# Kernel optimization log

Hardware: AMD Instinct MI355X
Metric: run time of the kernel (lower is better)

Reference implementation:

```python
import jax, jax.numpy as jnp
import numpy as np

B, H, L, DH = 4, 16, 2048, 64
EMBED_DIM = H * DH
CAUSAL = True


def setup_inputs() -> dict:
    key = jax.random.key(0)
    kq, kk, kv = jax.random.split(key, 3)
    return {
        "query": jax.random.normal(kq, (B, H, L, DH), dtype=jnp.float32),
        "key": jax.random.normal(kk, (B, H, L, DH), dtype=jnp.float32),
        "value": jax.random.normal(kv, (B, H, L, DH), dtype=jnp.float32),
    }


def reference(query, key, value):
    # scaled dot-product attention with causal mask, inputs [B, H, L, Dh]
    scale = 1.0 / jnp.sqrt(jnp.asarray(query.shape[-1], query.dtype))
    scores = jnp.einsum("bhld,bhsd->bhls", query, key) * scale  # [B,H,L,S]
    if CAUSAL:
        q_idx = jnp.arange(query.shape[-2])[:, None]
        k_idx = jnp.arange(key.shape[-2])[None, :]
        neg_inf = jnp.asarray(-jnp.inf, scores.dtype)
        scores = jnp.where(k_idx > q_idx, neg_inf, scores)
    attn = jax.nn.softmax(scores, axis=-1)
    out = jnp.einsum("bhls,bhsd->bhld", attn, value)  # [B,H,L,Dh]
    # merge heads -> [B, L, D]
    b = out.shape[0]
    return out.transpose(0, 2, 1, 3).reshape(b, -1, EMBED_DIM)
```

## Files before the change

kernel.cpp:

```cpp
#include <hip/hip_runtime.h>
#include <hip/hip_bf16.h>

#define B_   4
#define H_   16
#define L_   2048
#define DH_  64
#define QSCALE 0.1803368801111204f
#define LDK  72

typedef __bf16 bf16;
typedef __bf16 bf16x4 __attribute__((ext_vector_type(4)));
typedef __bf16 bf16x8 __attribute__((ext_vector_type(8)));
typedef float  f32x4  __attribute__((ext_vector_type(4)));

typedef const __attribute__((address_space(1))) unsigned int* gptr_t;
typedef __attribute__((address_space(3))) unsigned int* lptr_t;

__device__ __forceinline__ void load_lds16(const bf16* g, bf16* l) {
    __builtin_amdgcn_global_load_lds((gptr_t)(const void*)g, (lptr_t)(void*)l, 16, 0, 0);
}

__global__ __launch_bounds__(256, 4)
void prep(const float* __restrict__ K, const float* __restrict__ V,
          bf16* __restrict__ Kb, bf16* __restrict__ Vtg)
{
    __shared__ bf16 tl[64 * 72];
    const int t   = threadIdx.x;
    const int r   = t >> 2;
    const int c4  = t & 3;
    const int bid = blockIdx.x;
    const int kt  = bid & 31;
    const int bh  = bid >> 5;

    const float* Kp = K + ((size_t)bh * L_ + kt * 64) * DH_;
    const float* Vp = V + ((size_t)bh * L_ + kt * 64) * DH_;
    bf16* Kbp = Kb  + (size_t)bh * (L_ * DH_) + (size_t)(kt * 64) * DH_;
    bf16* Vtp = Vtg + (size_t)bh * (DH_ * L_) + kt * 64;

    {
        const float* src = Kp + r * DH_ + c4 * 16;
        f32x4 a = *(const f32x4*)(src);
        f32x4 b = *(const f32x4*)(src + 4);
        f32x4 c = *(const f32x4*)(src + 8);
        f32x4 d = *(const f32x4*)(src + 12);
        bf16x8 lo, hi;
        #pragma unroll
        for (int j = 0; j < 4; ++j) {
            lo[j] = (bf16)a[j]; lo[j + 4] = (bf16)b[j];
            hi[j] = (bf16)c[j]; hi[j + 4] = (bf16)d[j];
        }
        const int b0 = 2 * c4, b1 = 2 * c4 + 1;
        *(bf16x8*)(Kbp + r * 64 + (b0 ^ (r & 7)) * 8) = lo;
        *(bf16x8*)(Kbp + r * 64 + (b1 ^ (r & 7)) * 8) = hi;
    }
    {
        const float* src = Vp + r * DH_ + c4 * 16;
        f32x4 a = *(const f32x4*)(src);
        f32x4 b = *(const f32x4*)(src + 4);
        f32x4 c = *(const f32x4*)(src + 8);
        f32x4 d = *(const f32x4*)(src + 12);
        #pragma unroll
        for (int j = 0; j < 4; ++j) {
            tl[(c4 * 16 + j)      * 72 + r] = (bf16)a[j];
            tl[(c4 * 16 + 4 + j)  * 72 + r] = (bf16)b[j];
            tl[(c4 * 16 + 8 + j)  * 72 + r] = (bf16)c[j];
            tl[(c4 * 16 + 12 + j) * 72 + r] = (bf16)d[j];
        }
    }
    __syncthreads();
    {
        const int d = r;
        #pragma unroll
        for (int bi = 0; bi < 2; ++bi) {
            const int blk = 2 * c4 + bi;
            bf16x8 v;
            #pragma unroll
            for (int j = 0; j < 8; ++j) v[j] = tl[d * 72 + blk * 8 + j];
            *(bf16x8*)(Vtp + (size_t)d * L_ + (blk ^ (d & 7)) * 8) = v;
        }
    }
}

__global__ __launch_bounds__(256, 4)
void fa_fwd3(const float* __restrict__ Q, const bf16* __restrict__ Kb,
             const bf16* __restrict__ Vtg, float* __restrict__ O)
{
    __shared__ __align__(16) bf16 smem[2][2][64 * 64];
    __shared__ __align__(16) bf16 Pl[4][16 * 64];

    const int tid  = threadIdx.x;
    const int wave = tid >> 6;
    const int lane = tid & 63;
    const int quad = lane >> 4;
    const int l15  = lane & 15;

    const int u    = blockIdx.x;
    const int bh   = u & 63;
    const int s    = u >> 6;
    const int kq   = s >> 2;
    const int s0   = s & 3;
    const int base = ((kq & 1) == 0) ? (15 - (kq >> 1)) : (kq >> 1);
    const int Qt   = (kq & 1) ? (base + 2 * s0) : (base - 2 * s0);

    const int h    = bh & 15;
    const int b    = bh >> 4;

    const float* Qbh = Q + (size_t)bh * L_ * DH_;
    const bf16* Kbh  = Kb  + (size_t)bh * (L_ * DH_);
    const bf16* Vbh  = Vtg + (size_t)bh * (DH_ * L_);

    const int Rw = 16 * wave;
    const int lr = lane >> 3;
    const int lb = lane & 7;

    bf16x8 vone;
    #pragma unroll
    for (int jj = 0; jj < 8; ++jj) vone[jj] = (bf16)1.0f;

    int swb[2];
    #pragma unroll
    for (int ss = 0; ss < 2; ++ss) swb[ss] = ((4 * ss + quad) ^ (l15 & 7)) * 8;

    const int q0   = Qt * 128;
    const int jmax = 2 * Qt + 1;

    bf16x8 qf[2][2];
    #pragma unroll
    for (int qg = 0; qg < 2; ++qg) {
        const int row = q0 + 32 * wave + 16 * qg + l15;
        const float* qp = Qbh + (size_t)row * DH_ + quad * 8;
        #pragma unroll
        for (int ss = 0; ss < 2; ++ss) {
            f32x4 a = *(const f32x4*)(qp + ss * 32);
            f32x4 c = *(const f32x4*)(qp + ss * 32 + 4);
            #pragma unroll
            for (int jj = 0; jj < 4; ++jj) {
                qf[qg][ss][jj]     = (bf16)(a[jj] * QSCALE);
                qf[qg][ss][jj + 4] = (bf16)(c[jj] * QSCALE);
            }
        }
    }

    f32x4 o_acc[2][4];
    f32x4 l_acc[2];
    #pragma unroll
    for (int qg = 0; qg < 2; ++qg) {
        l_acc[qg] = (f32x4)0.0f;
        #pragma unroll
        for (int ct = 0; ct < 4; ++ct) o_acc[qg][ct] = (f32x4)0.0f;
    }

    {
        const bf16* kg = Kbh + (size_t)(Rw + lr) * 64 + lb * 8;
        const bf16* vg = Vbh + (size_t)(Rw + lr) * L_ + lb * 8;
        bf16* kl = &smem[0][0][Rw * 64];
        bf16* vl = &smem[0][1][Rw * 64];
        load_lds16(kg, kl);              load_lds16(kg + 8 * 64, kl + 8 * 64);
        load_lds16(vg, vl);              load_lds16(vg + (size_t)8 * L_, vl + 8 * 64);
    }

    for (int j = 0; j <= jmax; ++j) {
        __syncthreads();
        const int cur = j & 1;

        if (j < jmax) {
            const int nb  = cur ^ 1;
            const int kv0 = (j + 1) * 64;
            const bf16* kg = Kbh + (size_t)(kv0 + Rw + lr) * 64 + lb * 8;
            const bf16* vg = Vbh + (size_t)(Rw + lr) * L_ + kv0 + lb * 8;
            bf16* kl = &smem[nb][0][Rw * 64];
            bf16* vl = &smem[nb][1][Rw * 64];
            load_lds16(kg, kl);          load_lds16(kg + 8 * 64, kl + 8 * 64);
            load_lds16(vg, vl);          load_lds16(vg + (size_t)8 * L_, vl + 8 * 64);
        }

        const bool active = (j < 2 * Qt) || ((32 * wave + 31) >= ((j - 2 * Qt) << 6));
        if (active) {
            const bf16* Kl = smem[cur][0];
            const bf16* Vt = smem[cur][1];

            bf16x8 bk[4][2];
            #pragma unroll
            for (int ct = 0; ct < 4; ++ct)
                #pragma unroll
                for (int ss = 0; ss < 2; ++ss)
                    bk[ct][ss] = *(const bf16x8*)&Kl[(16 * ct + l15) * 64 + swb[ss]];

            bf16x8 pa[2][2];
            #pragma unroll
            for (int qg = 0; qg < 2; ++qg) {
                f32x4 sacc[4];
                #pragma unroll
                for (int ct = 0; ct < 4; ++ct) {
                    f32x4 acc = (f32x4)0.0f;
                    #pragma unroll
                    for (int ss = 0; ss < 2; ++ss)
                        acc = __builtin_amdgcn_mfma_f32_16x16x32_bf16(bk[ct][ss], qf[qg][ss], acc, 0, 0, 0);
                    sacc[ct] = acc;
                }

                if (j >= 2 * Qt) {
                    const int rlim = 32 * wave + 16 * qg + l15 - ((j - 2 * Qt) << 6);
                    #pragma unroll
                    for (int ct = 0; ct < 4; ++ct) {
                        #pragma unroll
                        for (int r = 0; r < 4; ++r)
                            if (16 * ct + quad * 4 + r > rlim) sacc[ct][r] = -1e30f;
                    }
                }

                #pragma unroll
                for (int ct = 0; ct < 4; ++ct) {
                    bf16x4 pk;
                    #pragma unroll
                    for (int r = 0; r < 4; ++r) pk[r] = (bf16)exp2f(sacc[ct][r]);
                    const int blk = 2 * ct + (quad >> 1);
                    *(bf16x4*)&Pl[wave][l15 * 64 + ((blk ^ (l15 & 7)) * 8) + (quad & 1) * 4] = pk;
                }
                #pragma unroll
                for (int ss = 0; ss < 2; ++ss)
                    pa[qg][ss] = *(const bf16x8*)&Pl[wave][l15 * 64 + swb[ss]];
            }

            #pragma unroll
            for (int ct = 0; ct < 4; ++ct) {
                #pragma unroll
                for (int ss = 0; ss < 2; ++ss) {
                    bf16x8 bv = *(const bf16x8*)&Vt[(16 * ct + l15) * 64 + swb[ss]];
                    #pragma unroll
                    for (int qg = 0; qg < 2; ++qg)
                        o_acc[qg][ct] = __builtin_amdgcn_mfma_f32_16x16x32_bf16(pa[qg][ss], bv, o_acc[qg][ct], 0, 0, 0);
                }
            }
            #pragma unroll
            for (int qg = 0; qg < 2; ++qg)
                #pragma unroll
                for (int ss = 0; ss < 2; ++ss)
                    l_acc[qg] = __builtin_amdgcn_mfma_f32_16x16x32_bf16(pa[qg][ss], vone, l_acc[qg], 0, 0, 0);
        }
    }

    #pragma unroll
    for (int qg = 0; qg < 2; ++qg)
        #pragma unroll
        for (int r = 0; r < 4; ++r) {
            const float inv = 1.0f / l_acc[qg][r];
            const int qrow = q0 + 32 * wave + 16 * qg + quad * 4 + r;
            float* op = &O[((size_t)b * L_ + qrow) * (H_ * DH_) + h * DH_];
            #pragma unroll
            for (int ct = 0; ct < 4; ++ct)
                op[16 * ct + l15] = o_acc[qg][ct][r] * inv;
        }
}

__global__ __launch_bounds__(256, 4)
void fa_fwd(const float* __restrict__ Q, const float* __restrict__ K,
            const float* __restrict__ V, float* __restrict__ O)
{
    __shared__ __align__(16) bf16 Kl[64 * LDK];
    __shared__ __align__(16) bf16 Vt[64 * LDK];
    __shared__ __align__(16) bf16 Pl[4][16 * LDK];

    const int tid  = threadIdx.x;
    const int wave = tid >> 6;
    const int lane = tid & 63;
    const int quad = lane >> 4;
    const int l15  = lane & 15;

    const int u    = blockIdx.x;
    const int xcd  = u & 7;
    const int p    = u >> 3;
    const int bh   = xcd * 8 + (p & 7);
    const int pidx = p >> 3;
    const int h    = bh & 15;
    const int b    = bh >> 4;

    const float* Qbh = Q + (size_t)bh * L_ * DH_;
    const float* Kbh = K + (size_t)bh * L_ * DH_;
    const float* Vbh = V + (size_t)bh * L_ * DH_;

    const int r0 = tid >> 4;
    const int c0 = (tid & 15) * 4;

    for (int pass = 0; pass < 2; ++pass) {
        const int qt = pass ? (31 - pidx) : pidx;
        const int q0 = qt * 64;

        bf16x8 qf[2];
        {
            const int row = q0 + wave * 16 + l15;
            const float* qp = Qbh + (size_t)row * DH_ + quad * 8;
            #pragma unroll
            for (int s = 0; s < 2; ++s) {
                f32x4 a = *(const f32x4*)(qp + s * 32);
                f32x4 c = *(const f32x4*)(qp + s * 32 + 4);
                #pragma unroll
                for (int jj = 0; jj < 4; ++jj) {
                    qf[s][jj]     = (bf16)(a[jj] * QSCALE);
                    qf[s][jj + 4] = (bf16)(c[jj] * QSCALE);
                }
            }
        }

        float m_run[4], l_run[4];
        f32x4 o_acc[4];
        #pragma unroll
        for (int r = 0; r < 4; ++r) { m_run[r] = -1e30f; l_run[r] = 0.0f; }
        #pragma unroll
        for (int ct = 0; ct < 4; ++ct) o_acc[ct] = (f32x4)0.0f;

        f32x4 kreg[4], vreg[4];
        #pragma unroll
        for (int i = 0; i < 4; ++i) {
            kreg[i] = *(const f32x4*)(Kbh + (size_t)(r0 + 16 * i) * DH_ + c0);
            vreg[i] = *(const f32x4*)(Vbh + (size_t)(r0 + 16 * i) * DH_ + c0);
        }

        for (int j = 0; j <= qt; ++j) {
            __syncthreads();
            #pragma unroll
            for (int i = 0; i < 4; ++i) {
                const int row = r0 + 16 * i;
                bf16x4 kb;
                #pragma unroll
                for (int c = 0; c < 4; ++c) kb[c] = (bf16)kreg[i][c];
                *(bf16x4*)&Kl[row * LDK + c0] = kb;
                Vt[(c0 + 0) * LDK + row] = (bf16)vreg[i][0];
                Vt[(c0 + 1) * LDK + row] = (bf16)vreg[i][1];
                Vt[(c0 + 2) * LDK + row] = (bf16)vreg[i][2];
                Vt[(c0 + 3) * LDK + row] = (bf16)vreg[i][3];
            }
            __syncthreads();

            if (j < qt) {
                const int kv0 = (j + 1) * 64;
                #pragma unroll
                for (int i = 0; i < 4; ++i) {
                    kreg[i] = *(const f32x4*)(Kbh + (size_t)(kv0 + r0 + 16 * i) * DH_ + c0);
                    vreg[i] = *(const f32x4*)(Vbh + (size_t)(kv0 + r0 + 16 * i) * DH_ + c0);
                }
            }

            f32x4 sacc[4];
            #pragma unroll
            for (int ct = 0; ct < 4; ++ct) {
                f32x4 acc = (f32x4)0.0f;
                #pragma unroll
                for (int s = 0; s < 2; ++s) {
                    bf16x8 bk = *(const bf16x8*)&Kl[(16 * ct + l15) * LDK + 32 * s + quad * 8];
                    acc = __builtin_amdgcn_mfma_f32_16x16x32_bf16(qf[s], bk, acc, 0, 0, 0);
                }
                sacc[ct] = acc;
            }

            if (j == qt) {
                #pragma unroll
                for (int ct = 0; ct < 4; ++ct) {
                    const int keyl = 16 * ct + l15;
                    #pragma unroll
                    for (int r = 0; r < 4; ++r)
                        if (keyl > wave * 16 + quad * 4 + r) sacc[ct][r] = -1e30f;
                }
            }

            #pragma unroll
            for (int r = 0; r < 4; ++r) {
                float mx = fmaxf(fmaxf(sacc[0][r], sacc[1][r]), fmaxf(sacc[2][r], sacc[3][r]));
                mx = fmaxf(mx, __shfl_xor(mx, 1));
                mx = fmaxf(mx, __shfl_xor(mx, 2));
                mx = fmaxf(mx, __shfl_xor(mx, 4));
                mx = fmaxf(mx, __shfl_xor(mx, 8));
                const float mnew  = fmaxf(m_run[r], mx);
                const float alpha = exp2f(m_run[r] - mnew);
                float sum = 0.0f;
                #pragma unroll
                for (int ct = 0; ct < 4; ++ct) {
                    const float pv = exp2f(sacc[ct][r] - mnew);
                    sacc[ct][r] = pv;
                    sum += pv;
                }
                sum += __shfl_xor(sum, 1);
                sum += __shfl_xor(sum, 2);
                sum += __shfl_xor(sum, 4);
                sum += __shfl_xor(sum, 8);
                l_run[r] = l_run[r] * alpha + sum;
                m_run[r] = mnew;
                #pragma unroll
                for (int ct = 0; ct < 4; ++ct) o_acc[ct][r] *= alpha;
            }

            #pragma unroll
            for (int ct = 0; ct < 4; ++ct)
                #pragma unroll
                for (int r = 0; r < 4; ++r)
                    Pl[wave][(quad * 4 + r) * LDK + 16 * ct + l15] = (bf16)sacc[ct][r];

            bf16x8 pa[2];
            #pragma unroll
            for (int s = 0; s < 2; ++s)
                pa[s] = *(const bf16x8*)&Pl[wave][l15 * LDK + 32 * s + quad * 8];

            #pragma unroll
            for (int ct = 0; ct < 4; ++ct)
                #pragma unroll
                for (int s = 0; s < 2; ++s) {
                    bf16x8 bv = *(const bf16x8*)&Vt[(16 * ct + l15) * LDK + 32 * s + quad * 8];
                    o_acc[ct] = __builtin_amdgcn_mfma_f32_16x16x32_bf16(pa[s], bv, o_acc[ct], 0, 0, 0);
                }
        }

        #pragma unroll
        for (int ct = 0; ct < 4; ++ct)
            #pragma unroll
            for (int r = 0; r < 4; ++r) {
                const int qrow = q0 + wave * 16 + quad * 4 + r;
                O[((size_t)b * L_ + qrow) * (H_ * DH_) + h * DH_ + (16 * ct + l15)] =
                    o_acc[ct][r] / l_run[r];
            }
    }
}

extern "C" void kernel_launch(void* const* d_in, const int* in_sizes, int n_in,
                              void* d_out, int out_size, void* d_ws, size_t ws_size,
                              hipStream_t stream) {
    const float* q = (const float*)d_in[0];
    const float* k = (const float*)d_in[1];
    const float* v = (const float*)d_in[2];
    float* out = (float*)d_out;
    const size_t need = 2ull * (size_t)(B_ * H_) * L_ * DH_ * sizeof(bf16);
    if (ws_size >= need) {
        bf16* Kb  = (bf16*)d_ws;
        bf16* Vtg = Kb + (size_t)(B_ * H_) * L_ * DH_;
        prep<<<dim3(B_ * H_ * (L_ / 64)), dim3(256), 0, stream>>>(k, v, Kb, Vtg);
        fa_fwd3<<<dim3(1024), dim3(256), 0, stream>>>(q, Kb, Vtg, out);
    } else {
        fa_fwd<<<dim3(B_ * H_ * 16), dim3(256), 0, stream>>>(q, k, v, out);
    }
}
```

Baseline: 194.6 us.

## Process paired 64-row query tiles per block for causal load balance

```diff
diff --git a/kernel.cpp b/kernel.cpp
--- a/kernel.cpp
+++ b/kernel.cpp
@@ -97,10 +97,6 @@
     const int u    = blockIdx.x;
     const int bh   = u & 63;
     const int s    = u >> 6;
-    const int kq   = s >> 2;
-    const int s0   = s & 3;
-    const int base = ((kq & 1) == 0) ? (15 - (kq >> 1)) : (kq >> 1);
-    const int Qt   = (kq & 1) ? (base + 2 * s0) : (base - 2 * s0);
 
     const int h    = bh & 15;
     const int b    = bh >> 4;
@@ -121,61 +117,56 @@
     #pragma unroll
     for (int ss = 0; ss < 2; ++ss) swb[ss] = ((4 * ss + quad) ^ (l15 & 7)) * 8;
 
-    const int q0   = Qt * 128;
-    const int jmax = 2 * Qt + 1;
-
-    bf16x8 qf[2][2];
-    #pragma unroll
-    for (int qg = 0; qg < 2; ++qg) {
-        const int row = q0 + 32 * wave + 16 * qg + l15;
-        const float* qp = Qbh + (size_t)row * DH_ + quad * 8;
-        #pragma unroll
-        for (int ss = 0; ss < 2; ++ss) {
-            f32x4 a = *(const f32x4*)(qp + ss * 32);
-            f32x4 c = *(const f32x4*)(qp + ss * 32 + 4);
-            #pragma unroll
-            for (int jj = 0; jj < 4; ++jj) {
-                qf[qg][ss][jj]     = (bf16)(a[jj] * QSCALE);
-                qf[qg][ss][jj + 4] = (bf16)(c[jj] * QSCALE);
-            }
-        }
-    }
-
-    f32x4 o_acc[2][4];
-    f32x4 l_acc[2];
-    #pragma unroll
-    for (int qg = 0; qg < 2; ++qg) {
-        l_acc[qg] = (f32x4)0.0f;
-        #pragma unroll
-        for (int ct = 0; ct < 4; ++ct) o_acc[qg][ct] = (f32x4)0.0f;
-    }
-
-    {
-        const bf16* kg = Kbh + (size_t)(Rw + lr) * 64 + lb * 8;
-        const bf16* vg = Vbh + (size_t)(Rw + lr) * L_ + lb * 8;
-        bf16* kl = &smem[0][0][Rw * 64];
-        bf16* vl = &smem[0][1][Rw * 64];
-        load_lds16(kg, kl);              load_lds16(kg + 8 * 64, kl + 8 * 64);
-        load_lds16(vg, vl);              load_lds16(vg + (size_t)8 * L_, vl + 8 * 64);
-    }
-
-    for (int j = 0; j <= jmax; ++j) {
-        __syncthreads();
-        const int cur = j & 1;
-
-        if (j < jmax) {
-            const int nb  = cur ^ 1;
-            const int kv0 = (j + 1) * 64;
-            const bf16* kg = Kbh + (size_t)(kv0 + Rw + lr) * 64 + lb * 8;
-            const bf16* vg = Vbh + (size_t)(Rw + lr) * L_ + kv0 + lb * 8;
-            bf16* kl = &smem[nb][0][Rw * 64];
-            bf16* vl = &smem[nb][1][Rw * 64];
-            load_lds16(kg, kl);          load_lds16(kg + 8 * 64, kl + 8 * 64);
-            load_lds16(vg, vl);          load_lds16(vg + (size_t)8 * L_, vl + 8 * 64);
-        }
-
-        const bool active = (j < 2 * Qt) || ((32 * wave + 31) >= ((j - 2 * Qt) << 6));
-        if (active) {
+    for (int pass = 0; pass < 2; ++pass) {
+        const int qt   = pass ? (31 - s) : s;
+        const int q0   = qt * 64;
+        const int jmax = qt;
+
+        bf16x8 qf[2];
+        {
+            const int row = q0 + 16 * wave + l15;
+            const float* qp = Qbh + (size_t)row * DH_ + quad * 8;
+            #pragma unroll
+            for (int ss = 0; ss < 2; ++ss) {
+                f32x4 a = *(const f32x4*)(qp + ss * 32);
+                f32x4 c = *(const f32x4*)(qp + ss * 32 + 4);
+                #pragma unroll
+                for (int jj = 0; jj < 4; ++jj) {
+                    qf[ss][jj]     = (bf16)(a[jj] * QSCALE);
+                    qf[ss][jj + 4] = (bf16)(c[jj] * QSCALE);
+                }
+            }
+        }
+
+        f32x4 o_acc[4];
+        f32x4 l_acc = (f32x4)0.0f;
+        #pragma unroll
+        for (int ct = 0; ct < 4; ++ct) o_acc[ct] = (f32x4)0.0f;
+
+        {
+            const bf16* kg = Kbh + (size_t)(Rw + lr) * 64 + lb * 8;
+            const bf16* vg = Vbh + (size_t)(Rw + lr) * L_ + lb * 8;
+            bf16* kl = &smem[0][0][Rw * 64];
+            bf16* vl = &smem[0][1][Rw * 64];
+            load_lds16(kg, kl);              load_lds16(kg + 8 * 64, kl + 8 * 64);
+            load_lds16(vg, vl);              load_lds16(vg + (size_t)8 * L_, vl + 8 * 64);
+        }
+
+        for (int j = 0; j <= jmax; ++j) {
+            __syncthreads();
+            const int cur = j & 1;
+
+            if (j < jmax) {
+                const int nb  = cur ^ 1;
+                const int kv0 = (j + 1) * 64;
+                const bf16* kg = Kbh + (size_t)(kv0 + Rw + lr) * 64 + lb * 8;
+                const bf16* vg = Vbh + (size_t)(Rw + lr) * L_ + kv0 + lb * 8;
+                bf16* kl = &smem[nb][0][Rw * 64];
+                bf16* vl = &smem[nb][1][Rw * 64];
+                load_lds16(kg, kl);          load_lds16(kg + 8 * 64, kl + 8 * 64);
+                load_lds16(vg, vl);          load_lds16(vg + (size_t)8 * L_, vl + 8 * 64);
+            }
+
             const bf16* Kl = smem[cur][0];
             const bf16* Vt = smem[cur][1];
 
@@ -186,71 +177,65 @@
                 for (int ss = 0; ss < 2; ++ss)
                     bk[ct][ss] = *(const bf16x8*)&Kl[(16 * ct + l15) * 64 + swb[ss]];
 
-            bf16x8 pa[2][2];
-            #pragma unroll
-            for (int qg = 0; qg < 2; ++qg) {
-                f32x4 sacc[4];
+            f32x4 sacc[4];
+            #pragma unroll
+            for (int ct = 0; ct < 4; ++ct) {
+                f32x4 acc = (f32x4)0.0f;
+                #pragma unroll
+                for (int ss = 0; ss < 2; ++ss)
+                    acc = __builtin_amdgcn_mfma_f32_16x16x32_bf16(bk[ct][ss], qf[ss], acc, 0, 0, 0);
+                sacc[ct] = acc;
+            }
+
+            if (j == jmax) {
+                const int rlim = 16 * wave + l15;
                 #pragma unroll
                 for (int ct = 0; ct < 4; ++ct) {
-                    f32x4 acc = (f32x4)0.0f;
                     #pragma unroll
-                    for (int ss = 0; ss < 2; ++ss)
-                        acc = __builtin_amdgcn_mfma_f32_16x16x32_bf16(bk[ct][ss], qf[qg][ss], acc, 0, 0, 0);
-                    sacc[ct] = acc;
-                }
-
-                if (j >= 2 * Qt) {
-                    const int rlim = 32 * wave + 16 * qg + l15 - ((j - 2 * Qt) << 6);
-                    #pragma unroll
-                    for (int ct = 0; ct < 4; ++ct) {
-                        #pragma unroll
-                        for (int r = 0; r < 4; ++r)
-                            if (16 * ct + quad * 4 + r > rlim) sacc[ct][r] = -1e30f;
-                    }
-                }
-
-                #pragma unroll
-                for (int ct = 0; ct < 4; ++ct) {
-                    bf16x4 pk;
-                    #pragma unroll
-                    for (int r = 0; r < 4; ++r) pk[r] = (bf16)exp2f(sacc[ct][r]);
-                    const int blk = 2 * ct + (quad >> 1);
-                    *(bf16x4*)&Pl[wave][l15 * 64 + ((blk ^ (l15 & 7)) * 8) + (quad & 1) * 4] = pk;
-                }
-                #pragma unroll
-                for (int ss = 0; ss < 2; ++ss)
-                    pa[qg][ss] = *(const bf16x8*)&Pl[wave][l15 * 64 + swb[ss]];
-            }
-
+                    for (int r = 0; r < 4; ++r)
+                        if (16 * ct + quad * 4 + r > rlim) sacc[ct][r] = -1e30f;
+                }
+            }
+
+            #pragma unroll
+            for (int ct = 0; ct < 4; ++ct) {
+                bf16x4 pk;
+                #pragma unroll
+                for (int r = 0; r < 4; ++r) pk[r] = (bf16)exp2f(sacc[ct][r]);
+                const int blk = 2 * ct + (quad >> 1);
+                *(bf16x4*)&Pl[wave][l15 * 64 + ((blk ^ (l15 & 7)) * 8) + (quad & 1) * 4] = pk;
+            }
+            bf16x8 pa[2];
+            #pragma unroll
+            for (int ss = 0; ss < 2; ++ss)
+                pa[ss] = *(const bf16x8*)&Pl[wave][l15 * 64 + swb[ss]];
+
+            __builtin_amdgcn_s_setprio(1);
             #pragma unroll
             for (int ct = 0; ct < 4; ++ct) {
                 #pragma unroll
                 for (int ss = 0; ss < 2; ++ss) {
                     bf16x8 bv = *(const bf16x8*)&Vt[(16 * ct + l15) * 64 + swb[ss]];
-                    #pragma unroll
-                    for (int qg = 0; qg < 2; ++qg)
-                        o_acc[qg][ct] = __builtin_amdgcn_mfma_f32_16x16x32_bf16(pa[qg][ss], bv, o_acc[qg][ct], 0, 0, 0);
-                }
-            }
-            #pragma unroll
-            for (int qg = 0; qg < 2; ++qg)
-                #pragma unroll
-                for (int ss = 0; ss < 2; ++ss)
-                    l_acc[qg] = __builtin_amdgcn_mfma_f32_16x16x32_bf16(pa[qg][ss], vone, l_acc[qg], 0, 0, 0);
-        }
-    }
-
-    #pragma unroll
-    for (int qg = 0; qg < 2; ++qg)
+                    o_acc[ct] = __builtin_amdgcn_mfma_f32_16x16x32_bf16(pa[ss], bv, o_acc[ct], 0, 0, 0);
+                }
+            }
+            #pragma unroll
+            for (int ss = 0; ss < 2; ++ss)
+                l_acc = __builtin_amdgcn_mfma_f32_16x16x32_bf16(pa[ss], vone, l_acc, 0, 0, 0);
+            __builtin_amdgcn_s_setprio(0);
+        }
+        __syncthreads();
+
         #pragma unroll
         for (int r = 0; r < 4; ++r) {
-            const float inv = 1.0f / l_acc[qg][r];
-            const int qrow = q0 + 32 * wave + 16 * qg + quad * 4 + r;
+            const float inv = 1.0f / l_acc[r];
+            const int qrow = q0 + 16 * wave + quad * 4 + r;
             float* op = &O[((size_t)b * L_ + qrow) * (H_ * DH_) + h * DH_];
             #pragma unroll
             for (int ct = 0; ct < 4; ++ct)
-                op[16 * ct + l15] = o_acc[qg][ct][r] * inv;
-        }
+                op[16 * ct + l15] = o_acc[ct][r] * inv;
+        }
+    }
 }
 
 __global__ __launch_bounds__(256, 4)
```

Measured after the change: 188.1 us. -3.4%, faster.

## Pair causal Q tiles per block and software-pipeline PV MFMAs across iterations

Applied to the files above, without the earlier changes.

```diff
diff --git a/kernel.cpp b/kernel.cpp
--- a/kernel.cpp
+++ b/kernel.cpp
@@ -81,7 +81,7 @@
     }
 }
 
-__global__ __launch_bounds__(256, 4)
+__global__ __launch_bounds__(256, 2)
 void fa_fwd3(const float* __restrict__ Q, const bf16* __restrict__ Kb,
              const bf16* __restrict__ Vtg, float* __restrict__ O)
 {
@@ -95,12 +95,10 @@
     const int l15  = lane & 15;
 
     const int u    = blockIdx.x;
-    const int bh   = u & 63;
-    const int s    = u >> 6;
-    const int kq   = s >> 2;
-    const int s0   = s & 3;
-    const int base = ((kq & 1) == 0) ? (15 - (kq >> 1)) : (kq >> 1);
-    const int Qt   = (kq & 1) ? (base + 2 * s0) : (base - 2 * s0);
+    const int xcd  = u & 7;
+    const int t    = u >> 3;
+    const int bh   = xcd * 8 + (t & 7);
+    const int pidx = t >> 3;
 
     const int h    = bh & 15;
     const int b    = bh >> 4;
@@ -121,61 +119,64 @@
     #pragma unroll
     for (int ss = 0; ss < 2; ++ss) swb[ss] = ((4 * ss + quad) ^ (l15 & 7)) * 8;
 
-    const int q0   = Qt * 128;
-    const int jmax = 2 * Qt + 1;
-
-    bf16x8 qf[2][2];
-    #pragma unroll
-    for (int qg = 0; qg < 2; ++qg) {
-        const int row = q0 + 32 * wave + 16 * qg + l15;
-        const float* qp = Qbh + (size_t)row * DH_ + quad * 8;
-        #pragma unroll
-        for (int ss = 0; ss < 2; ++ss) {
-            f32x4 a = *(const f32x4*)(qp + ss * 32);
-            f32x4 c = *(const f32x4*)(qp + ss * 32 + 4);
-            #pragma unroll
-            for (int jj = 0; jj < 4; ++jj) {
-                qf[qg][ss][jj]     = (bf16)(a[jj] * QSCALE);
-                qf[qg][ss][jj + 4] = (bf16)(c[jj] * QSCALE);
-            }
-        }
-    }
-
-    f32x4 o_acc[2][4];
-    f32x4 l_acc[2];
-    #pragma unroll
-    for (int qg = 0; qg < 2; ++qg) {
-        l_acc[qg] = (f32x4)0.0f;
-        #pragma unroll
-        for (int ct = 0; ct < 4; ++ct) o_acc[qg][ct] = (f32x4)0.0f;
-    }
-
-    {
-        const bf16* kg = Kbh + (size_t)(Rw + lr) * 64 + lb * 8;
-        const bf16* vg = Vbh + (size_t)(Rw + lr) * L_ + lb * 8;
-        bf16* kl = &smem[0][0][Rw * 64];
-        bf16* vl = &smem[0][1][Rw * 64];
-        load_lds16(kg, kl);              load_lds16(kg + 8 * 64, kl + 8 * 64);
-        load_lds16(vg, vl);              load_lds16(vg + (size_t)8 * L_, vl + 8 * 64);
-    }
-
-    for (int j = 0; j <= jmax; ++j) {
-        __syncthreads();
-        const int cur = j & 1;
-
-        if (j < jmax) {
-            const int nb  = cur ^ 1;
-            const int kv0 = (j + 1) * 64;
-            const bf16* kg = Kbh + (size_t)(kv0 + Rw + lr) * 64 + lb * 8;
-            const bf16* vg = Vbh + (size_t)(Rw + lr) * L_ + kv0 + lb * 8;
-            bf16* kl = &smem[nb][0][Rw * 64];
-            bf16* vl = &smem[nb][1][Rw * 64];
-            load_lds16(kg, kl);          load_lds16(kg + 8 * 64, kl + 8 * 64);
-            load_lds16(vg, vl);          load_lds16(vg + (size_t)8 * L_, vl + 8 * 64);
-        }
-
-        const bool active = (j < 2 * Qt) || ((32 * wave + 31) >= ((j - 2 * Qt) << 6));
-        if (active) {
+    for (int pass = 0; pass < 2; ++pass) {
+        const int Qt   = pass ? (15 - pidx) : pidx;
+        const int q0   = Qt * 128;
+        const int jmax = 2 * Qt + 1;
+
+        bf16x8 qf[2][2];
+        #pragma unroll
+        for (int qg = 0; qg < 2; ++qg) {
+            const int row = q0 + 32 * wave + 16 * qg + l15;
+            const float* qp = Qbh + (size_t)row * DH_ + quad * 8;
+            #pragma unroll
+            for (int ss = 0; ss < 2; ++ss) {
+                f32x4 a = *(const f32x4*)(qp + ss * 32);
+                f32x4 c = *(const f32x4*)(qp + ss * 32 + 4);
+                #pragma unroll
+                for (int jj = 0; jj < 4; ++jj) {
+                    qf[qg][ss][jj]     = (bf16)(a[jj] * QSCALE);
+                    qf[qg][ss][jj + 4] = (bf16)(c[jj] * QSCALE);
+                }
+            }
+        }
+
+        f32x4 o_acc[2][4];
+        f32x4 l_acc[2];
+        #pragma unroll
+        for (int qg = 0; qg < 2; ++qg) {
+            l_acc[qg] = (f32x4)0.0f;
+            #pragma unroll
+            for (int ct = 0; ct < 4; ++ct) o_acc[qg][ct] = (f32x4)0.0f;
+        }
+
+        bf16x8 pa[2][2];
+        bf16x8 bvp[4][2];
+
+        {
+            const bf16* kg = Kbh + (size_t)(Rw + lr) * 64 + lb * 8;
+            const bf16* vg = Vbh + (size_t)(Rw + lr) * L_ + lb * 8;
+            bf16* kl = &smem[0][0][Rw * 64];
+            bf16* vl = &smem[0][1][Rw * 64];
+            load_lds16(kg, kl);              load_lds16(kg + 8 * 64, kl + 8 * 64);
+            load_lds16(vg, vl);              load_lds16(vg + (size_t)8 * L_, vl + 8 * 64);
+        }
+
+        for (int j = 0; j <= jmax; ++j) {
+            __syncthreads();
+            const int cur = j & 1;
+
+            if (j < jmax) {
+                const int nb  = cur ^ 1;
+                const int kv0 = (j + 1) * 64;
+                const bf16* kg = Kbh + (size_t)(kv0 + Rw + lr) * 64 + lb * 8;
+                const bf16* vg = Vbh + (size_t)(Rw + lr) * L_ + kv0 + lb * 8;
+                bf16* kl = &smem[nb][0][Rw * 64];
+                bf16* vl = &smem[nb][1][Rw * 64];
+                load_lds16(kg, kl);          load_lds16(kg + 8 * 64, kl + 8 * 64);
+                load_lds16(vg, vl);          load_lds16(vg + (size_t)8 * L_, vl + 8 * 64);
+            }
+
             const bf16* Kl = smem[cur][0];
             const bf16* Vt = smem[cur][1];
 
@@ -186,7 +187,29 @@
                 for (int ss = 0; ss < 2; ++ss)
                     bk[ct][ss] = *(const bf16x8*)&Kl[(16 * ct + l15) * 64 + swb[ss]];
 
-            bf16x8 pa[2][2];
+            if (j > 0) {
+                __builtin_amdgcn_s_setprio(1);
+                #pragma unroll
+                for (int ct = 0; ct < 4; ++ct)
+                    #pragma unroll
+                    for (int ss = 0; ss < 2; ++ss)
+                        #pragma unroll
+                        for (int qg = 0; qg < 2; ++qg)
+                            o_acc[qg][ct] = __builtin_amdgcn_mfma_f32_16x16x32_bf16(pa[qg][ss], bvp[ct][ss], o_acc[qg][ct], 0, 0, 0);
+                #pragma unroll
+                for (int qg = 0; qg < 2; ++qg)
+                    #pragma unroll
+                    for (int ss = 0; ss < 2; ++ss)
+                        l_acc[qg] = __builtin_amdgcn_mfma_f32_16x16x32_bf16(pa[qg][ss], vone, l_acc[qg], 0, 0, 0);
+                __builtin_amdgcn_s_setprio(0);
+            }
+
+            #pragma unroll
+            for (int ct = 0; ct < 4; ++ct)
+                #pragma unroll
+                for (int ss = 0; ss < 2; ++ss)
+                    bvp[ct][ss] = *(const bf16x8*)&Vt[(16 * ct + l15) * 64 + swb[ss]];
+
             #pragma unroll
             for (int qg = 0; qg < 2; ++qg) {
                 f32x4 sacc[4];
@@ -221,36 +244,37 @@
                 for (int ss = 0; ss < 2; ++ss)
                     pa[qg][ss] = *(const bf16x8*)&Pl[wave][l15 * 64 + swb[ss]];
             }
-
-            #pragma unroll
-            for (int ct = 0; ct < 4; ++ct) {
-                #pragma unroll
-                for (int ss = 0; ss < 2; ++ss) {
-                    bf16x8 bv = *(const bf16x8*)&Vt[(16 * ct + l15) * 64 + swb[ss]];
-                    #pragma unroll
-                    for (int qg = 0; qg < 2; ++qg)
-                        o_acc[qg][ct] = __builtin_amdgcn_mfma_f32_16x16x32_bf16(pa[qg][ss], bv, o_acc[qg][ct], 0, 0, 0);
-                }
-            }
-            #pragma unroll
-            for (int qg = 0; qg < 2; ++qg)
-                #pragma unroll
-                for (int ss = 0; ss < 2; ++ss)
-                    l_acc[qg] = __builtin_amdgcn_mfma_f32_16x16x32_bf16(pa[qg][ss], vone, l_acc[qg], 0, 0, 0);
-        }
-    }
-
-    #pragma unroll
-    for (int qg = 0; qg < 2; ++qg)
-        #pragma unroll
-        for (int r = 0; r < 4; ++r) {
-            const float inv = 1.0f / l_acc[qg][r];
-            const int qrow = q0 + 32 * wave + 16 * qg + quad * 4 + r;
-            float* op = &O[((size_t)b * L_ + qrow) * (H_ * DH_) + h * DH_];
-            #pragma unroll
-            for (int ct = 0; ct < 4; ++ct)
-                op[16 * ct + l15] = o_acc[qg][ct][r] * inv;
-        }
+        }
+
+        __builtin_amdgcn_s_setprio(1);
+        #pragma unroll
+        for (int ct = 0; ct < 4; ++ct)
+            #pragma unroll
+            for (int ss = 0; ss < 2; ++ss)
+                #pragma unroll
+                for (int qg = 0; qg < 2; ++qg)
+                    o_acc[qg][ct] = __builtin_amdgcn_mfma_f32_16x16x32_bf16(pa[qg][ss], bvp[ct][ss], o_acc[qg][ct], 0, 0, 0);
+        #pragma unroll
+        for (int qg = 0; qg < 2; ++qg)
+            #pragma unroll
+            for (int ss = 0; ss < 2; ++ss)
+                l_acc[qg] = __builtin_amdgcn_mfma_f32_16x16x32_bf16(pa[qg][ss], vone, l_acc[qg], 0, 0, 0);
+        __builtin_amdgcn_s_setprio(0);
+
+        __syncthreads();
+
+        #pragma unroll
+        for (int qg = 0; qg < 2; ++qg)
+            #pragma unroll
+            for (int r = 0; r < 4; ++r) {
+                const float inv = 1.0f / l_acc[qg][r];
+                const int qrow = q0 + 32 * wave + 16 * qg + quad * 4 + r;
+                float* op = &O[((size_t)b * L_ + qrow) * (H_ * DH_) + h * DH_];
+                #pragma unroll
+                for (int ct = 0; ct < 4; ++ct)
+                    op[16 * ct + l15] = o_acc[qg][ct][r] * inv;
+            }
+    }
 }
 
 __global__ __launch_bounds__(256, 4)
@@ -432,7 +456,7 @@
         bf16* Kb  = (bf16*)d_ws;
         bf16* Vtg = Kb + (size_t)(B_ * H_) * L_ * DH_;
         prep<<<dim3(B_ * H_ * (L_ / 64)), dim3(256), 0, stream>>>(k, v, Kb, Vtg);
-        fa_fwd3<<<dim3(1024), dim3(256), 0, stream>>>(q, Kb, Vtg, out);
+        fa_fwd3<<<dim3(512), dim3(256), 0, stream>>>(q, Kb, Vtg, out);
     } else {
         fa_fwd<<<dim3(B_ * H_ * 16), dim3(256), 0, stream>>>(q, k, v, out);
     }
```

Measured after the change: 190.8 us. 2.0% less time.

## Pair complementary causal q-tiles per block and stage two KV tiles per barrier

Applied to the files above, without the earlier changes.

```diff
diff --git a/kernel.cpp b/kernel.cpp
--- a/kernel.cpp
+++ b/kernel.cpp
@@ -81,11 +81,11 @@
     }
 }
 
-__global__ __launch_bounds__(256, 4)
+__global__ __launch_bounds__(256, 2)
 void fa_fwd3(const float* __restrict__ Q, const bf16* __restrict__ Kb,
              const bf16* __restrict__ Vtg, float* __restrict__ O)
 {
-    __shared__ __align__(16) bf16 smem[2][2][64 * 64];
+    __shared__ __align__(16) bf16 smem[4][2][64 * 64];
     __shared__ __align__(16) bf16 Pl[4][16 * 64];
 
     const int tid  = threadIdx.x;
@@ -95,12 +95,10 @@
     const int l15  = lane & 15;
 
     const int u    = blockIdx.x;
-    const int bh   = u & 63;
-    const int s    = u >> 6;
-    const int kq   = s >> 2;
-    const int s0   = s & 3;
-    const int base = ((kq & 1) == 0) ? (15 - (kq >> 1)) : (kq >> 1);
-    const int Qt   = (kq & 1) ? (base + 2 * s0) : (base - 2 * s0);
+    const int xcd  = u & 7;
+    const int t    = u >> 3;
+    const int bh   = xcd * 8 + (t & 7);
+    const int pidx = t >> 3;
 
     const int h    = bh & 15;
     const int b    = bh >> 4;
@@ -121,63 +119,48 @@
     #pragma unroll
     for (int ss = 0; ss < 2; ++ss) swb[ss] = ((4 * ss + quad) ^ (l15 & 7)) * 8;
 
-    const int q0   = Qt * 128;
-    const int jmax = 2 * Qt + 1;
-
-    bf16x8 qf[2][2];
-    #pragma unroll
-    for (int qg = 0; qg < 2; ++qg) {
-        const int row = q0 + 32 * wave + 16 * qg + l15;
-        const float* qp = Qbh + (size_t)row * DH_ + quad * 8;
-        #pragma unroll
-        for (int ss = 0; ss < 2; ++ss) {
-            f32x4 a = *(const f32x4*)(qp + ss * 32);
-            f32x4 c = *(const f32x4*)(qp + ss * 32 + 4);
-            #pragma unroll
-            for (int jj = 0; jj < 4; ++jj) {
-                qf[qg][ss][jj]     = (bf16)(a[jj] * QSCALE);
-                qf[qg][ss][jj + 4] = (bf16)(c[jj] * QSCALE);
-            }
-        }
-    }
-
-    f32x4 o_acc[2][4];
-    f32x4 l_acc[2];
-    #pragma unroll
-    for (int qg = 0; qg < 2; ++qg) {
-        l_acc[qg] = (f32x4)0.0f;
-        #pragma unroll
-        for (int ct = 0; ct < 4; ++ct) o_acc[qg][ct] = (f32x4)0.0f;
-    }
-
-    {
-        const bf16* kg = Kbh + (size_t)(Rw + lr) * 64 + lb * 8;
-        const bf16* vg = Vbh + (size_t)(Rw + lr) * L_ + lb * 8;
-        bf16* kl = &smem[0][0][Rw * 64];
-        bf16* vl = &smem[0][1][Rw * 64];
+    auto stage = [&](int kv0, int slot) {
+        const bf16* kg = Kbh + (size_t)(kv0 + Rw + lr) * 64 + lb * 8;
+        const bf16* vg = Vbh + (size_t)(Rw + lr) * L_ + kv0 + lb * 8;
+        bf16* kl = &smem[slot][0][Rw * 64];
+        bf16* vl = &smem[slot][1][Rw * 64];
         load_lds16(kg, kl);              load_lds16(kg + 8 * 64, kl + 8 * 64);
         load_lds16(vg, vl);              load_lds16(vg + (size_t)8 * L_, vl + 8 * 64);
-    }
-
-    for (int j = 0; j <= jmax; ++j) {
-        __syncthreads();
-        const int cur = j & 1;
-
-        if (j < jmax) {
-            const int nb  = cur ^ 1;
-            const int kv0 = (j + 1) * 64;
-            const bf16* kg = Kbh + (size_t)(kv0 + Rw + lr) * 64 + lb * 8;
-            const bf16* vg = Vbh + (size_t)(Rw + lr) * L_ + kv0 + lb * 8;
-            bf16* kl = &smem[nb][0][Rw * 64];
-            bf16* vl = &smem[nb][1][Rw * 64];
-            load_lds16(kg, kl);          load_lds16(kg + 8 * 64, kl + 8 * 64);
-            load_lds16(vg, vl);          load_lds16(vg + (size_t)8 * L_, vl + 8 * 64);
-        }
-
-        const bool active = (j < 2 * Qt) || ((32 * wave + 31) >= ((j - 2 * Qt) << 6));
-        if (active) {
-            const bf16* Kl = smem[cur][0];
-            const bf16* Vt = smem[cur][1];
+    };
+
+    for (int pass = 0; pass < 2; ++pass) {
+        const int Qt   = pass ? (15 - pidx) : pidx;
+        const int q0   = Qt * 128;
+
+        bf16x8 qf[2][2];
+        #pragma unroll
+        for (int qg = 0; qg < 2; ++qg) {
+            const int row = q0 + 32 * wave + 16 * qg + l15;
+            const float* qp = Qbh + (size_t)row * DH_ + quad * 8;
+            #pragma unroll
+            for (int ss = 0; ss < 2; ++ss) {
+                f32x4 a = *(const f32x4*)(qp + ss * 32);
+                f32x4 c = *(const f32x4*)(qp + ss * 32 + 4);
+                #pragma unroll
+                for (int jj = 0; jj < 4; ++jj) {
+                    qf[qg][ss][jj]     = (bf16)(a[jj] * QSCALE);
+                    qf[qg][ss][jj + 4] = (bf16)(c[jj] * QSCALE);
+                }
+            }
+        }
+
+        f32x4 o_acc[2][4];
+        f32x4 l_acc[2];
+        #pragma unroll
+        for (int qg = 0; qg < 2; ++qg) {
+            l_acc[qg] = (f32x4)0.0f;
+            #pragma unroll
+            for (int ct = 0; ct < 4; ++ct) o_acc[qg][ct] = (f32x4)0.0f;
+        }
+
+        auto compute_tile = [&](int slot, int moff) {
+            const bf16* Kl = smem[slot][0];
+            const bf16* Vt = smem[slot][1];
 
             bf16x8 bk[4][2];
             #pragma unroll
@@ -199,8 +182,8 @@
                     sacc[ct] = acc;
                 }
 
-                if (j >= 2 * Qt) {
-                    const int rlim = 32 * wave + 16 * qg + l15 - ((j - 2 * Qt) << 6);
+                if (moff >= 0) {
+                    const int rlim = 32 * wave + 16 * qg + l15 - moff;
                     #pragma unroll
                     for (int ct = 0; ct < 4; ++ct) {
                         #pragma unroll
@@ -222,6 +205,7 @@
                     pa[qg][ss] = *(const bf16x8*)&Pl[wave][l15 * 64 + swb[ss]];
             }
 
+            __builtin_amdgcn_s_setprio(1);
             #pragma unroll
             for (int ct = 0; ct < 4; ++ct) {
                 #pragma unroll
@@ -237,20 +221,40 @@
                 #pragma unroll
                 for (int ss = 0; ss < 2; ++ss)
                     l_acc[qg] = __builtin_amdgcn_mfma_f32_16x16x32_bf16(pa[qg][ss], vone, l_acc[qg], 0, 0, 0);
-        }
-    }
-
-    #pragma unroll
-    for (int qg = 0; qg < 2; ++qg)
-        #pragma unroll
-        for (int r = 0; r < 4; ++r) {
-            const float inv = 1.0f / l_acc[qg][r];
-            const int qrow = q0 + 32 * wave + 16 * qg + quad * 4 + r;
-            float* op = &O[((size_t)b * L_ + qrow) * (H_ * DH_) + h * DH_];
-            #pragma unroll
-            for (int ct = 0; ct < 4; ++ct)
-                op[16 * ct + l15] = o_acc[qg][ct][r] * inv;
-        }
+            __builtin_amdgcn_s_setprio(0);
+        };
+
+        stage(0, 0);
+        stage(64, 1);
+
+        const int npair = Qt + 1;
+        for (int p = 0; p < npair; ++p) {
+            __syncthreads();
+
+            if (p + 1 < npair) {
+                stage((2 * p + 2) * 64, (2 * p + 2) & 3);
+                stage((2 * p + 3) * 64, (2 * p + 3) & 3);
+            }
+
+            const bool diag = (p == Qt);
+            compute_tile((2 * p) & 3, diag ? 0 : -1);
+            if (!diag || wave >= 2)
+                compute_tile((2 * p + 1) & 3, diag ? 64 : -1);
+        }
+        __syncthreads();
+
+        #pragma unroll
+        for (int qg = 0; qg < 2; ++qg)
+            #pragma unroll
+            for (int r = 0; r < 4; ++r) {
+                const float inv = 1.0f / l_acc[qg][r];
+                const int qrow = q0 + 32 * wave + 16 * qg + quad * 4 + r;
+                float* op = &O[((size_t)b * L_ + qrow) * (H_ * DH_) + h * DH_];
+                #pragma unroll
+                for (int ct = 0; ct < 4; ++ct)
+                    op[16 * ct + l15] = o_acc[qg][ct][r] * inv;
+            }
+    }
 }
 
 __global__ __launch_bounds__(256, 4)
@@ -432,7 +436,7 @@
         bf16* Kb  = (bf16*)d_ws;
         bf16* Vtg = Kb + (size_t)(B_ * H_) * L_ * DH_;
         prep<<<dim3(B_ * H_ * (L_ / 64)), dim3(256), 0, stream>>>(k, v, Kb, Vtg);
-        fa_fwd3<<<dim3(1024), dim3(256), 0, stream>>>(q, Kb, Vtg, out);
+        fa_fwd3<<<dim3(512), dim3(256), 0, stream>>>(q, Kb, Vtg, out);
     } else {
         fa_fwd<<<dim3(B_ * H_ * 16), dim3(256), 0, stream>>>(q, k, v, out);
     }
```

Result: no change. 192.0 us (-1.4%).
